# Kernel tuning notes

Hardware: AMD Instinct MI355X
Metric: run time of the kernel (lower is better)

Reference implementation:

```python
import jax, jax.numpy as jnp
import numpy as np

N, D = 16384, 64


def setup_inputs() -> dict:
    key = jax.random.key(0)
    k1, k2, k3, k4, k5 = jax.random.split(key, 5)
    x = jax.random.normal(k1, (N, D), dtype=jnp.float32)
    # labels in {-1, +1}
    y = jnp.sign(jax.random.normal(k2, (N,), dtype=jnp.float32))
    y = jnp.where(y == 0, 1.0, y)
    alpha = jax.random.uniform(k3, (N, 1), dtype=jnp.float32)
    xi = jax.random.uniform(k4, (N, 1), dtype=jnp.float32)
    b = jax.random.uniform(k5, (1,), dtype=jnp.float32, minval=-1.0, maxval=1.0)
    return {"x": x, "y": y, "alpha": alpha, "xi": xi, "b": b,
            "coeff": 1, "degree": 3, "C": 1, "lambd": 1}


def reference(x, y, alpha, xi, b, coeff, degree, C, lambd):
    a = jax.nn.relu(alpha)          # (N,1)
    xr = jax.nn.relu(xi)            # (N,1)
    # polynomial kernel Gram matrix: (x @ x.T + coeff)^degree  -> (N,N)
    K = (x @ x.T + coeff) ** degree
    # sum_j alpha_j * y_j * K_ij  (weighted row reduction)
    s = K @ (a * y[:, None])        # (N,1)
    left = y[:, None] * (s + b)     # (N,1)
    right = 1.0 - xr                # (N,1)
    loss = (0.5 * jnp.sum(jnp.abs(a))
            + C * jnp.sum(xr)
            + lambd * jnp.mean(left - right))
    return loss
```

## Files before the change

kernel.cpp:

```cpp
#include <hip/hip_runtime.h>

#define N_SAMP 16384
#define D_FEAT 64
#define TILE 128
#define NTILE 128
#define SPLIT 8
#define NPAIR (NTILE / 2)
#define NBLOCKS (NPAIR * SPLIT)
#define TPP (NTILE + 1)
#define SEG_BASE (TPP / SPLIT)
#define SEG_REM (TPP % SPLIT)

typedef __attribute__((ext_vector_type(8))) short bf16x8;
typedef __attribute__((ext_vector_type(4))) float f32x4;
typedef __attribute__((ext_vector_type(2))) float f32x2;
typedef __attribute__((ext_vector_type(4))) unsigned short u16x4;

typedef __attribute__((address_space(3))) unsigned lds_u32_t;
typedef const __attribute__((address_space(1))) unsigned glb_u32_t;

__device__ __forceinline__ void load16_to_lds(const void* g, void* l) {
  __builtin_amdgcn_global_load_lds((glb_u32_t*)g, (lds_u32_t*)l, 16, 0, 0);
}

__device__ __forceinline__ unsigned short f2bf_rne(float f) {
  union { float f; unsigned u; } v;
  v.f = f;
  unsigned u = v.u;
  return (unsigned short)((u + 0x7FFFu + ((u >> 16) & 1u)) >> 16);
}

__global__ __launch_bounds__(256) void prep_kernel(
    const float* __restrict__ x, const float* __restrict__ y,
    const float* __restrict__ alpha, const float* __restrict__ xi,
    unsigned short* __restrict__ xb, float4* __restrict__ psums) {
  int t = blockIdx.x * 256 + threadIdx.x;
  int base = t * 4;
  int row = base >> 6;
  float yv = y[row];
  float4 v = *(const float4*)(x + base);
  u16x4 o;
  o.x = f2bf_rne(v.x * yv);
  o.y = f2bf_rne(v.y * yv);
  o.z = f2bf_rne(v.z * yv);
  o.w = f2bf_rne(v.w * yv);
  *(u16x4*)(xb + base) = o;

  if (blockIdx.x < (N_SAMP / 256)) {
    float a = fmaxf(alpha[t], 0.0f);
    float xr = fmaxf(xi[t], 0.0f);
    float yy = y[t];
#pragma unroll
    for (int off = 32; off > 0; off >>= 1) {
      a += __shfl_down(a, off, 64);
      xr += __shfl_down(xr, off, 64);
      yy += __shfl_down(yy, off, 64);
    }
    __shared__ float ra[4], rx[4], ry[4];
    int wv = threadIdx.x >> 6;
    if ((threadIdx.x & 63) == 0) {
      ra[wv] = a;
      rx[wv] = xr;
      ry[wv] = yy;
    }
    __syncthreads();
    if (threadIdx.x == 0)
      psums[blockIdx.x] =
          make_float4(ra[0] + ra[1] + ra[2] + ra[3],
                      rx[0] + rx[1] + rx[2] + rx[3],
                      ry[0] + ry[1] + ry[2] + ry[3], 0.0f);
  }
}

__global__ __launch_bounds__(256, 2) void tile_kernel(
    const unsigned short* __restrict__ xb,
    const float* __restrict__ alpha,
    const float* __restrict__ y,
    const int* __restrict__ coeffp,
    const int* __restrict__ degp,
    float* __restrict__ partials) {
  __shared__ unsigned short smB[4][2][64 * 64];
  __shared__ float wred[4];

  const int tid = threadIdx.x;
  const int lane = tid & 63;
  const int wv = tid >> 6;
  const int wm = wv >> 1;
  const int wn = wv & 1;
  const int lr = lane & 15;
  const int q = lane >> 4;

  const int p = blockIdx.x >> 3;
  const int sb = blockIdx.x & (SPLIT - 1);
  const int i1 = p, i2 = NTILE - 1 - p;
  const int cnt1 = NTILE - p;
  const int g0 = sb * SEG_BASE + (sb < SEG_REM ? sb : SEG_REM);
  const int gcnt = SEG_BASE + (sb < SEG_REM ? 1 : 0);

  const char* xbytes = (const char*)xb;
  char* mybuf = (char*)smB + (wv << 14);

  const float fco = (float)coeffp[0];
  const int deg = degp[0];

  const int swz =
      ((lane >> 3) << 7) + (((lane & 7) ^ ((lane >> 3) & 7)) << 4);

  auto stage_wave = [&](int coltile, int k) {
    const char* gbase =
        xbytes + (((size_t)(coltile * TILE + wn * 64)) << 7) + swz;
    char* dst = mybuf + (k << 13);
#pragma unroll
    for (int L = 0; L < 8; ++L)
      load16_to_lds(gbase + (L << 10), dst + (L << 10));
  };

  f32x2 yr[4][2], ar[4][2];
  auto load_rows = [&](int ic) {
#pragma unroll
    for (int mt = 0; mt < 4; ++mt) {
      int idx = ic * TILE + wm * 64 + mt * 16 + q * 4;
      float4 yv = *(const float4*)(y + idx);
      float4 av = *(const float4*)(alpha + idx);
      yr[mt][0] = (f32x2){yv.x, yv.y};
      yr[mt][1] = (f32x2){yv.z, yv.w};
      ar[mt][0] = (f32x2){fmaxf(av.x, 0.0f), fmaxf(av.y, 0.0f)};
      ar[mt][1] = (f32x2){fmaxf(av.z, 0.0f), fmaxf(av.w, 0.0f)};
    }
  };

  bf16x8 af[4][2];
  auto read_af_g = [&](int rowtile) {
    const char* base = xbytes + (((size_t)(rowtile * TILE + wm * 64)) << 7);
#pragma unroll
    for (int mt = 0; mt < 4; ++mt) {
      int r = mt * 16 + lr;
#pragma unroll
      for (int kc = 0; kc < 2; ++kc)
        af[mt][kc] = *(const bf16x8*)(base + (r << 7) + ((kc * 4 + q) << 4));
    }
  };

  f32x2 rsum[4][2];
#pragma unroll
  for (int mt = 0; mt < 4; ++mt)
    for (int h = 0; h < 2; ++h) rsum[mt][h] = (f32x2){0.0f, 0.0f};
  float lane_total = 0.0f;

  auto flush_rsum = [&]() {
#pragma unroll
    for (int mt = 0; mt < 4; ++mt) {
      f32x2 s = rsum[mt][0] * ar[mt][0] + rsum[mt][1] * ar[mt][1];
      lane_total += s.x + s.y;
      rsum[mt][0] = (f32x2){0.0f, 0.0f};
      rsum[mt][1] = (f32x2){0.0f, 0.0f};
    }
  };

  int jfirst = (g0 < cnt1) ? (p + g0) : (i2 + (g0 - cnt1));
  stage_wave(jfirst, 0);
  int icur = (g0 < cnt1) ? i1 : i2;
  load_rows(icur);
  read_af_g(icur);

  for (int it = 0; it < gcnt; ++it) {
    int g = g0 + it;
    int i = (g < cnt1) ? i1 : i2;
    int j = (g < cnt1) ? (p + g) : (i2 + (g - cnt1));
    char* bufc = mybuf + ((it & 1) << 13);

    if (i != icur) {
      flush_rsum();
      load_rows(i);
      read_af_g(i);
      icur = i;
    }

    float ycol[4], wcol[4];
#pragma unroll
    for (int nt = 0; nt < 4; ++nt) {
      int jj = j * TILE + wn * 64 + nt * 16 + lr;
      ycol[nt] = y[jj];
      wcol[nt] = fmaxf(alpha[jj], 0.0f);
    }

    if (it + 1 < gcnt) {
      int gn = g + 1;
      int jn = (gn < cnt1) ? (p + gn) : (i2 + (gn - cnt1));
      stage_wave(jn, (it + 1) & 1);
      __builtin_amdgcn_s_waitcnt(0x0F78);
    } else {
      __builtin_amdgcn_s_waitcnt(0x0F70);
    }

    f32x4 acc[4][4];
#pragma unroll
    for (int mt = 0; mt < 4; ++mt) {
#pragma unroll
      for (int nt = 0; nt < 4; ++nt) {
        float s = ycol[nt] * fco;
        f32x2 lo = yr[mt][0] * s;
        f32x2 hi = yr[mt][1] * s;
        acc[mt][nt][0] = lo.x;
        acc[mt][nt][1] = lo.y;
        acc[mt][nt][2] = hi.x;
        acc[mt][nt][3] = hi.y;
      }
    }

#pragma unroll
    for (int kc = 0; kc < 2; ++kc) {
      bf16x8 bfr[4];
#pragma unroll
      for (int nt = 0; nt < 4; ++nt) {
        int rr = nt * 16 + lr;
        bfr[nt] = *(const bf16x8*)(bufc + (rr << 7) +
                                   (((kc * 4 + q) ^ (rr & 7)) << 4));
      }
#pragma unroll
      for (int mt = 0; mt < 4; ++mt) {
#pragma unroll
        for (int nt = 0; nt < 4; ++nt) {
          acc[mt][nt] = __builtin_amdgcn_mfma_f32_16x16x32_bf16(
              af[mt][kc], bfr[nt], acc[mt][nt], 0, 0, 0);
        }
      }
    }

    bool diagonal = (j == i);
    if (deg == 3) {
      if (diagonal) {
#pragma unroll
        for (int nt = 0; nt < 4; ++nt) {
          f32x2 cs = {0.0f, 0.0f};
#pragma unroll
          for (int mt = 0; mt < 4; ++mt) {
#pragma unroll
            for (int h = 0; h < 2; ++h) {
              f32x2 T = {acc[mt][nt][2 * h], acc[mt][nt][2 * h + 1]};
              f32x2 T2 = T * T;
              cs += T2 * T;
            }
          }
          lane_total = fmaf(cs.x + cs.y, wcol[nt], lane_total);
        }
      } else {
#pragma unroll
        for (int nt = 0; nt < 4; ++nt) {
          f32x2 cs = {0.0f, 0.0f};
#pragma unroll
          for (int mt = 0; mt < 4; ++mt) {
#pragma unroll
            for (int h = 0; h < 2; ++h) {
              f32x2 T = {acc[mt][nt][2 * h], acc[mt][nt][2 * h + 1]};
              f32x2 T2 = T * T;
              f32x2 P = T2 * T;
              cs += P;
              rsum[mt][h] += P;
            }
          }
          lane_total = fmaf(cs.x + cs.y, wcol[nt], lane_total);
        }
      }
    } else {
#pragma unroll
      for (int nt = 0; nt < 4; ++nt) {
        float cs = 0.0f;
#pragma unroll
        for (int mt = 0; mt < 4; ++mt) {
          float ys[4] = {yr[mt][0].x, yr[mt][0].y, yr[mt][1].x, yr[mt][1].y};
          float as[4] = {ar[mt][0].x, ar[mt][0].y, ar[mt][1].x, ar[mt][1].y};
#pragma unroll
          for (int rg = 0; rg < 4; ++rg) {
            float T = acc[mt][nt][rg];
            float pw = 1.0f;
            for (int d = 0; d < deg; ++d) pw *= T;
            if (!(deg & 1)) pw *= ys[rg] * ycol[nt];
            cs += pw;
            if (!diagonal) lane_total += pw * as[rg];
          }
        }
        lane_total = fmaf(cs, wcol[nt], lane_total);
      }
    }
  }

  flush_rsum();

#pragma unroll
  for (int off = 32; off > 0; off >>= 1)
    lane_total += __shfl_down(lane_total, off, 64);
  if (lane == 0) wred[wv] = lane_total;
  __syncthreads();
  if (tid == 0)
    partials[blockIdx.x] = wred[0] + wred[1] + wred[2] + wred[3];
}

__global__ __launch_bounds__(256) void finalize_kernel(
    const float* __restrict__ partials,
    const float4* __restrict__ psums,
    const float* __restrict__ bp,
    const int* __restrict__ Cp,
    const int* __restrict__ lamp,
    float* __restrict__ out) {
  double tsum = 0.0, sa = 0.0, sx = 0.0, sy = 0.0;
  for (int i = threadIdx.x; i < NBLOCKS; i += 256) tsum += (double)partials[i];
  if (threadIdx.x < (N_SAMP / 256)) {
    float4 v = psums[threadIdx.x];
    sa = (double)v.x;
    sx = (double)v.y;
    sy = (double)v.z;
  }
#pragma unroll
  for (int off = 32; off > 0; off >>= 1) {
    tsum += __shfl_down(tsum, off, 64);
    sa += __shfl_down(sa, off, 64);
    sx += __shfl_down(sx, off, 64);
    sy += __shfl_down(sy, off, 64);
  }
  __shared__ double red[4][4];
  int wv = threadIdx.x >> 6;
  if ((threadIdx.x & 63) == 0) {
    red[wv][0] = tsum;
    red[wv][1] = sa;
    red[wv][2] = sx;
    red[wv][3] = sy;
  }
  __syncthreads();
  if (threadIdx.x == 0) {
    double T = red[0][0] + red[1][0] + red[2][0] + red[3][0];
    double A = red[0][1] + red[1][1] + red[2][1] + red[3][1];
    double X = red[0][2] + red[1][2] + red[2][2] + red[3][2];
    double Y = red[0][3] + red[1][3] + red[2][3] + red[3][3];
    double b = (double)bp[0];
    double Cc = (double)Cp[0];
    double lam = (double)lamp[0];
    double mean = (T + b * Y - (double)N_SAMP + X) / (double)N_SAMP;
    out[0] = (float)(0.5 * A + Cc * X + lam * mean);
  }
}

extern "C" void kernel_launch(void* const* d_in, const int* in_sizes, int n_in,
                              void* d_out, int out_size, void* d_ws,
                              size_t ws_size, hipStream_t stream) {
  const float* x = (const float*)d_in[0];
  const float* y = (const float*)d_in[1];
  const float* alpha = (const float*)d_in[2];
  const float* xi = (const float*)d_in[3];
  const float* b = (const float*)d_in[4];
  const int* coeff = (const int*)d_in[5];
  const int* degree = (const int*)d_in[6];
  const int* C = (const int*)d_in[7];
  const int* lambd = (const int*)d_in[8];

  unsigned short* xb = (unsigned short*)d_ws;
  char* pbase = (char*)d_ws + (size_t)N_SAMP * D_FEAT * 2;
  float* partials = (float*)pbase;
  float4* psums = (float4*)(pbase + ((NBLOCKS * 4 + 255) & ~255));

  prep_kernel<<<(N_SAMP * D_FEAT) / (4 * 256), 256, 0, stream>>>(x, y, alpha,
                                                                 xi, xb, psums);

  tile_kernel<<<NBLOCKS, 256, 0, stream>>>(xb, alpha, y, coeff, degree,
                                           partials);

  finalize_kernel<<<1, 256, 0, stream>>>(partials, psums, b, C, lambd,
                                         (float*)d_out);
}
```

Baseline: 107.4 us.

## Fuse prep, tile and finalize kernels into one cooperative grid-synced kernel

After: 313.7 us. +192.2%, slower.

```diff
diff --git a/kernel.cpp b/kernel.cpp
--- a/kernel.cpp
+++ b/kernel.cpp
@@ -1,4 +1,7 @@
 #include <hip/hip_runtime.h>
+#include <hip/hip_cooperative_groups.h>
+
+namespace cg = cooperative_groups;
 
 #define N_SAMP 16384
 #define D_FEAT 64
@@ -28,6 +31,321 @@
   v.f = f;
   unsigned u = v.u;
   return (unsigned short)((u + 0x7FFFu + ((u >> 16) & 1u)) >> 16);
+}
+
+__global__ __launch_bounds__(256, 2) void fused_kernel(
+    const float* __restrict__ x, const float* __restrict__ y,
+    const float* __restrict__ alpha, const float* __restrict__ xi,
+    const float* __restrict__ bp, const int* __restrict__ coeffp,
+    const int* __restrict__ degp, const int* __restrict__ Cp,
+    const int* __restrict__ lamp, unsigned short* __restrict__ xb,
+    float4* __restrict__ psums, float* __restrict__ partials,
+    float* __restrict__ out) {
+  __shared__ unsigned short smB[4][2][64 * 64];
+  __shared__ float wred[4];
+  __shared__ float rtrip[3][4];
+  __shared__ double red[4][4];
+
+  const int tid = threadIdx.x;
+  const int bid = blockIdx.x;
+
+  {
+#pragma unroll
+    for (int half = 0; half < 2; ++half) {
+      int t = half * (NBLOCKS * 256) + bid * 256 + tid;
+      int base = t * 4;
+      int row = base >> 6;
+      float yv = y[row];
+      float4 v = *(const float4*)(x + base);
+      u16x4 o;
+      o.x = f2bf_rne(v.x * yv);
+      o.y = f2bf_rne(v.y * yv);
+      o.z = f2bf_rne(v.z * yv);
+      o.w = f2bf_rne(v.w * yv);
+      *(u16x4*)(xb + base) = o;
+    }
+    if (bid < (N_SAMP / 256)) {
+      int t = bid * 256 + tid;
+      float a = fmaxf(alpha[t], 0.0f);
+      float xr = fmaxf(xi[t], 0.0f);
+      float yy = y[t];
+#pragma unroll
+      for (int off = 32; off > 0; off >>= 1) {
+        a += __shfl_down(a, off, 64);
+        xr += __shfl_down(xr, off, 64);
+        yy += __shfl_down(yy, off, 64);
+      }
+      int wv = tid >> 6;
+      if ((tid & 63) == 0) {
+        rtrip[0][wv] = a;
+        rtrip[1][wv] = xr;
+        rtrip[2][wv] = yy;
+      }
+      __syncthreads();
+      if (tid == 0)
+        psums[bid] = make_float4(
+            rtrip[0][0] + rtrip[0][1] + rtrip[0][2] + rtrip[0][3],
+            rtrip[1][0] + rtrip[1][1] + rtrip[1][2] + rtrip[1][3],
+            rtrip[2][0] + rtrip[2][1] + rtrip[2][2] + rtrip[2][3], 0.0f);
+    }
+  }
+
+  __threadfence();
+  cg::this_grid().sync();
+
+  {
+    const int lane = tid & 63;
+    const int wv = tid >> 6;
+    const int wm = wv >> 1;
+    const int wn = wv & 1;
+    const int lr = lane & 15;
+    const int q = lane >> 4;
+
+    const int p = bid >> 3;
+    const int sb = bid & (SPLIT - 1);
+    const int i1 = p, i2 = NTILE - 1 - p;
+    const int cnt1 = NTILE - p;
+    const int g0 = sb * SEG_BASE + (sb < SEG_REM ? sb : SEG_REM);
+    const int gcnt = SEG_BASE + (sb < SEG_REM ? 1 : 0);
+
+    const char* xbytes = (const char*)xb;
+    char* mybuf = (char*)smB + (wv << 14);
+
+    const float fco = (float)coeffp[0];
+    const int deg = degp[0];
+
+    const int swz =
+        ((lane >> 3) << 7) + (((lane & 7) ^ ((lane >> 3) & 7)) << 4);
+
+    auto stage_wave = [&](int coltile, int k) {
+      const char* gbase =
+          xbytes + (((size_t)(coltile * TILE + wn * 64)) << 7) + swz;
+      char* dst = mybuf + (k << 13);
+#pragma unroll
+      for (int L = 0; L < 8; ++L)
+        load16_to_lds(gbase + (L << 10), dst + (L << 10));
+    };
+
+    f32x2 yr[4][2], ar[4][2];
+    auto load_rows = [&](int ic) {
+#pragma unroll
+      for (int mt = 0; mt < 4; ++mt) {
+        int idx = ic * TILE + wm * 64 + mt * 16 + q * 4;
+        float4 yv = *(const float4*)(y + idx);
+        float4 av = *(const float4*)(alpha + idx);
+        yr[mt][0] = (f32x2){yv.x, yv.y};
+        yr[mt][1] = (f32x2){yv.z, yv.w};
+        ar[mt][0] = (f32x2){fmaxf(av.x, 0.0f), fmaxf(av.y, 0.0f)};
+        ar[mt][1] = (f32x2){fmaxf(av.z, 0.0f), fmaxf(av.w, 0.0f)};
+      }
+    };
+
+    bf16x8 af[4][2];
+    auto read_af_g = [&](int rowtile) {
+      const char* base = xbytes + (((size_t)(rowtile * TILE + wm * 64)) << 7);
+#pragma unroll
+      for (int mt = 0; mt < 4; ++mt) {
+        int r = mt * 16 + lr;
+#pragma unroll
+        for (int kc = 0; kc < 2; ++kc)
+          af[mt][kc] = *(const bf16x8*)(base + (r << 7) + ((kc * 4 + q) << 4));
+      }
+    };
+
+    f32x2 rsum[4][2];
+#pragma unroll
+    for (int mt = 0; mt < 4; ++mt)
+      for (int h = 0; h < 2; ++h) rsum[mt][h] = (f32x2){0.0f, 0.0f};
+    float lane_total = 0.0f;
+
+    auto flush_rsum = [&]() {
+#pragma unroll
+      for (int mt = 0; mt < 4; ++mt) {
+        f32x2 s = rsum[mt][0] * ar[mt][0] + rsum[mt][1] * ar[mt][1];
+        lane_total += s.x + s.y;
+        rsum[mt][0] = (f32x2){0.0f, 0.0f};
+        rsum[mt][1] = (f32x2){0.0f, 0.0f};
+      }
+    };
+
+    int jfirst = (g0 < cnt1) ? (p + g0) : (i2 + (g0 - cnt1));
+    stage_wave(jfirst, 0);
+    int icur = (g0 < cnt1) ? i1 : i2;
+    load_rows(icur);
+    read_af_g(icur);
+
+    for (int it = 0; it < gcnt; ++it) {
+      int g = g0 + it;
+      int i = (g < cnt1) ? i1 : i2;
+      int j = (g < cnt1) ? (p + g) : (i2 + (g - cnt1));
+      char* bufc = mybuf + ((it & 1) << 13);
+
+      if (i != icur) {
+        flush_rsum();
+        load_rows(i);
+        read_af_g(i);
+        icur = i;
+      }
+
+      float ycol[4], wcol[4];
+#pragma unroll
+      for (int nt = 0; nt < 4; ++nt) {
+        int jj = j * TILE + wn * 64 + nt * 16 + lr;
+        ycol[nt] = y[jj];
+        wcol[nt] = fmaxf(alpha[jj], 0.0f);
+      }
+
+      if (it + 1 < gcnt) {
+        int gn = g + 1;
+        int jn = (gn < cnt1) ? (p + gn) : (i2 + (gn - cnt1));
+        stage_wave(jn, (it + 1) & 1);
+        __builtin_amdgcn_s_waitcnt(0x0F78);
+      } else {
+        __builtin_amdgcn_s_waitcnt(0x0F70);
+      }
+
+      f32x4 acc[4][4];
+#pragma unroll
+      for (int mt = 0; mt < 4; ++mt) {
+#pragma unroll
+        for (int nt = 0; nt < 4; ++nt) {
+          float s = ycol[nt] * fco;
+          f32x2 lo = yr[mt][0] * s;
+          f32x2 hi = yr[mt][1] * s;
+          acc[mt][nt][0] = lo.x;
+          acc[mt][nt][1] = lo.y;
+          acc[mt][nt][2] = hi.x;
+          acc[mt][nt][3] = hi.y;
+        }
+      }
+
+#pragma unroll
+      for (int kc = 0; kc < 2; ++kc) {
+        bf16x8 bfr[4];
+#pragma unroll
+        for (int nt = 0; nt < 4; ++nt) {
+          int rr = nt * 16 + lr;
+          bfr[nt] = *(const bf16x8*)(bufc + (rr << 7) +
+                                     (((kc * 4 + q) ^ (rr & 7)) << 4));
+        }
+#pragma unroll
+        for (int mt = 0; mt < 4; ++mt) {
+#pragma unroll
+          for (int nt = 0; nt < 4; ++nt) {
+            acc[mt][nt] = __builtin_amdgcn_mfma_f32_16x16x32_bf16(
+                af[mt][kc], bfr[nt], acc[mt][nt], 0, 0, 0);
+          }
+        }
+      }
+
+      bool diagonal = (j == i);
+      if (deg == 3) {
+        if (diagonal) {
+#pragma unroll
+          for (int nt = 0; nt < 4; ++nt) {
+            f32x2 cs = {0.0f, 0.0f};
+#pragma unroll
+            for (int mt = 0; mt < 4; ++mt) {
+#pragma unroll
+              for (int h = 0; h < 2; ++h) {
+                f32x2 T = {acc[mt][nt][2 * h], acc[mt][nt][2 * h + 1]};
+                f32x2 T2 = T * T;
+                cs += T2 * T;
+              }
+            }
+            lane_total = fmaf(cs.x + cs.y, wcol[nt], lane_total);
+          }
+        } else {
+#pragma unroll
+          for (int nt = 0; nt < 4; ++nt) {
+            f32x2 cs = {0.0f, 0.0f};
+#pragma unroll
+            for (int mt = 0; mt < 4; ++mt) {
+#pragma unroll
+              for (int h = 0; h < 2; ++h) {
+                f32x2 T = {acc[mt][nt][2 * h], acc[mt][nt][2 * h + 1]};
+                f32x2 T2 = T * T;
+                f32x2 P = T2 * T;
+                cs += P;
+                rsum[mt][h] += P;
+              }
+            }
+            lane_total = fmaf(cs.x + cs.y, wcol[nt], lane_total);
+          }
+        }
+      } else {
+#pragma unroll
+        for (int nt = 0; nt < 4; ++nt) {
+          float cs = 0.0f;
+#pragma unroll
+          for (int mt = 0; mt < 4; ++mt) {
+            float ys[4] = {yr[mt][0].x, yr[mt][0].y, yr[mt][1].x, yr[mt][1].y};
+            float as[4] = {ar[mt][0].x, ar[mt][0].y, ar[mt][1].x, ar[mt][1].y};
+#pragma unroll
+            for (int rg = 0; rg < 4; ++rg) {
+              float T = acc[mt][nt][rg];
+              float pw = 1.0f;
+              for (int d = 0; d < deg; ++d) pw *= T;
+              if (!(deg & 1)) pw *= ys[rg] * ycol[nt];
+              cs += pw;
+              if (!diagonal) lane_total += pw * as[rg];
+            }
+          }
+          lane_total = fmaf(cs, wcol[nt], lane_total);
+        }
+      }
+    }
+
+    flush_rsum();
+
+#pragma unroll
+    for (int off = 32; off > 0; off >>= 1)
+      lane_total += __shfl_down(lane_total, off, 64);
+    if (lane == 0) wred[wv] = lane_total;
+    __syncthreads();
+    if (tid == 0)
+      partials[bid] = wred[0] + wred[1] + wred[2] + wred[3];
+  }
+
+  __threadfence();
+  cg::this_grid().sync();
+
+  if (bid == 0) {
+    double tsum = 0.0, sa = 0.0, sx = 0.0, sy = 0.0;
+    for (int i = tid; i < NBLOCKS; i += 256) tsum += (double)partials[i];
+    if (tid < (N_SAMP / 256)) {
+      float4 v = psums[tid];
+      sa = (double)v.x;
+      sx = (double)v.y;
+      sy = (double)v.z;
+    }
+#pragma unroll
+    for (int off = 32; off > 0; off >>= 1) {
+      tsum += __shfl_down(tsum, off, 64);
+      sa += __shfl_down(sa, off, 64);
+      sx += __shfl_down(sx, off, 64);
+      sy += __shfl_down(sy, off, 64);
+    }
+    int wv = tid >> 6;
+    if ((tid & 63) == 0) {
+      red[wv][0] = tsum;
+      red[wv][1] = sa;
+      red[wv][2] = sx;
+      red[wv][3] = sy;
+    }
+    __syncthreads();
+    if (tid == 0) {
+      double T = red[0][0] + red[1][0] + red[2][0] + red[3][0];
+      double A = red[0][1] + red[1][1] + red[2][1] + red[3][1];
+      double X = red[0][2] + red[1][2] + red[2][2] + red[3][2];
+      double Y = red[0][3] + red[1][3] + red[2][3] + red[3][3];
+      double b = (double)bp[0];
+      double Cc = (double)Cp[0];
+      double lam = (double)lamp[0];
+      double mean = (T + b * Y - (double)N_SAMP + X) / (double)N_SAMP;
+      out[0] = (float)(0.5 * A + Cc * X + lam * mean);
+    }
+  }
 }
 
 __global__ __launch_bounds__(256) void prep_kernel(
@@ -357,13 +675,22 @@
   char* pbase = (char*)d_ws + (size_t)N_SAMP * D_FEAT * 2;
   float* partials = (float*)pbase;
   float4* psums = (float4*)(pbase + ((NBLOCKS * 4 + 255) & ~255));
-
-  prep_kernel<<<(N_SAMP * D_FEAT) / (4 * 256), 256, 0, stream>>>(x, y, alpha,
-                                                                 xi, xb, psums);
-
-  tile_kernel<<<NBLOCKS, 256, 0, stream>>>(xb, alpha, y, coeff, degree,
-                                           partials);
-
-  finalize_kernel<<<1, 256, 0, stream>>>(partials, psums, b, C, lambd,
-                                         (float*)d_out);
+  float* out = (float*)d_out;
+
+  void* args[] = {(void*)&x,     (void*)&y,      (void*)&alpha,
+                  (void*)&xi,    (void*)&b,      (void*)&coeff,
+                  (void*)&degree,(void*)&C,      (void*)&lambd,
+                  (void*)&xb,    (void*)&psums,  (void*)&partials,
+                  (void*)&out};
+  hipError_t err = hipLaunchCooperativeKernel(
+      (const void*)fused_kernel, dim3(NBLOCKS), dim3(256), (void**)args, 0,
+      stream);
+
+  if (err != hipSuccess) {
+    prep_kernel<<<(N_SAMP * D_FEAT) / (4 * 256), 256, 0, stream>>>(
+        x, y, alpha, xi, xb, psums);
+    tile_kernel<<<NBLOCKS, 256, 0, stream>>>(xb, alpha, y, coeff, degree,
+                                             partials);
+    finalize_kernel<<<1, 256, 0, stream>>>(partials, psums, b, C, lambd, out);
+  }
 }
```

## Prefetch next column labels/weights and stagger tile order across block halves

Applied to the files above, without the earlier changes.

Result: no change. 106.0 us, median of 2 (-1.2%).

```diff
diff --git a/kernel.cpp b/kernel.cpp
--- a/kernel.cpp
+++ b/kernel.cpp
@@ -97,6 +97,22 @@
   const int g0 = sb * SEG_BASE + (sb < SEG_REM ? sb : SEG_REM);
   const int gcnt = SEG_BASE + (sb < SEG_REM ? 1 : 0);
 
+  const int ph = ((blockIdx.x >> 8) & 1) * (gcnt >> 1);
+  auto map_g = [&](int it) {
+    int gg = it + ph;
+    if (gg >= gcnt) gg -= gcnt;
+    return g0 + gg;
+  };
+  auto g_to_ij = [&](int g, int& i, int& j) {
+    if (g < cnt1) {
+      i = i1;
+      j = p + g;
+    } else {
+      i = i2;
+      j = i2 + (g - cnt1);
+    }
+  };
+
   const char* xbytes = (const char*)xb;
   char* mybuf = (char*)smB + (wv << 14);
 
@@ -157,16 +173,25 @@
     }
   };
 
-  int jfirst = (g0 < cnt1) ? (p + g0) : (i2 + (g0 - cnt1));
+  int gfirst = map_g(0);
+  int icur, jfirst;
+  g_to_ij(gfirst, icur, jfirst);
   stage_wave(jfirst, 0);
-  int icur = (g0 < cnt1) ? i1 : i2;
+
+  float ycol[4], wcol[4];
+#pragma unroll
+  for (int nt = 0; nt < 4; ++nt) {
+    int jj = jfirst * TILE + wn * 64 + nt * 16 + lr;
+    ycol[nt] = y[jj];
+    wcol[nt] = fmaxf(alpha[jj], 0.0f);
+  }
   load_rows(icur);
   read_af_g(icur);
 
   for (int it = 0; it < gcnt; ++it) {
-    int g = g0 + it;
-    int i = (g < cnt1) ? i1 : i2;
-    int j = (g < cnt1) ? (p + g) : (i2 + (g - cnt1));
+    int g = map_g(it);
+    int i, j;
+    g_to_ij(g, i, j);
     char* bufc = mybuf + ((it & 1) << 13);
 
     if (i != icur) {
@@ -176,31 +201,40 @@
       icur = i;
     }
 
-    float ycol[4], wcol[4];
-#pragma unroll
-    for (int nt = 0; nt < 4; ++nt) {
-      int jj = j * TILE + wn * 64 + nt * 16 + lr;
-      ycol[nt] = y[jj];
-      wcol[nt] = fmaxf(alpha[jj], 0.0f);
-    }
-
-    if (it + 1 < gcnt) {
-      int gn = g + 1;
-      int jn = (gn < cnt1) ? (p + gn) : (i2 + (gn - cnt1));
+    int jnext = 0;
+    bool have_next = (it + 1 < gcnt);
+    if (have_next) {
+      int gn = map_g(it + 1);
+      int in_, jn;
+      g_to_ij(gn, in_, jn);
+      jnext = jn;
       stage_wave(jn, (it + 1) & 1);
       __builtin_amdgcn_s_waitcnt(0x0F78);
     } else {
       __builtin_amdgcn_s_waitcnt(0x0F70);
     }
 
+    float ycol_n[4], wraw_n[4];
+    if (have_next) {
+#pragma unroll
+      for (int nt = 0; nt < 4; ++nt) {
+        int jj = jnext * TILE + wn * 64 + nt * 16 + lr;
+        ycol_n[nt] = y[jj];
+        wraw_n[nt] = alpha[jj];
+      }
+    }
+
+    float ysc[4];
+#pragma unroll
+    for (int nt = 0; nt < 4; ++nt) ysc[nt] = ycol[nt] * fco;
+
     f32x4 acc[4][4];
 #pragma unroll
     for (int mt = 0; mt < 4; ++mt) {
 #pragma unroll
       for (int nt = 0; nt < 4; ++nt) {
-        float s = ycol[nt] * fco;
-        f32x2 lo = yr[mt][0] * s;
-        f32x2 hi = yr[mt][1] * s;
+        f32x2 lo = yr[mt][0] * ysc[nt];
+        f32x2 hi = yr[mt][1] * ysc[nt];
         acc[mt][nt][0] = lo.x;
         acc[mt][nt][1] = lo.y;
         acc[mt][nt][2] = hi.x;
@@ -281,6 +315,14 @@
           }
         }
         lane_total = fmaf(cs, wcol[nt], lane_total);
+      }
+    }
+
+    if (have_next) {
+#pragma unroll
+      for (int nt = 0; nt < 4; ++nt) {
+        ycol[nt] = ycol_n[nt];
+        wcol[nt] = fmaxf(wraw_n[nt], 0.0f);
       }
     }
   }
```

## Load B fragments straight from global and overlap previous tile's epilogue

Applied to the files above, without the earlier changes.

After: 111.0 us. 1.03x slower.

```diff
diff --git a/kernel.cpp b/kernel.cpp
--- a/kernel.cpp
+++ b/kernel.cpp
@@ -15,13 +15,6 @@
 typedef __attribute__((ext_vector_type(4))) float f32x4;
 typedef __attribute__((ext_vector_type(2))) float f32x2;
 typedef __attribute__((ext_vector_type(4))) unsigned short u16x4;
-
-typedef __attribute__((address_space(3))) unsigned lds_u32_t;
-typedef const __attribute__((address_space(1))) unsigned glb_u32_t;
-
-__device__ __forceinline__ void load16_to_lds(const void* g, void* l) {
-  __builtin_amdgcn_global_load_lds((glb_u32_t*)g, (lds_u32_t*)l, 16, 0, 0);
-}
 
 __device__ __forceinline__ unsigned short f2bf_rne(float f) {
   union { float f; unsigned u; } v;
@@ -79,7 +72,6 @@
     const int* __restrict__ coeffp,
     const int* __restrict__ degp,
     float* __restrict__ partials) {
-  __shared__ unsigned short smB[4][2][64 * 64];
   __shared__ float wred[4];
 
   const int tid = threadIdx.x;
@@ -97,23 +89,19 @@
   const int g0 = sb * SEG_BASE + (sb < SEG_REM ? sb : SEG_REM);
   const int gcnt = SEG_BASE + (sb < SEG_REM ? 1 : 0);
 
+  auto g_to_ij = [&](int g, int& i, int& j) {
+    if (g < cnt1) {
+      i = i1;
+      j = p + g;
+    } else {
+      i = i2;
+      j = i2 + (g - cnt1);
+    }
+  };
+
   const char* xbytes = (const char*)xb;
-  char* mybuf = (char*)smB + (wv << 14);
-
   const float fco = (float)coeffp[0];
   const int deg = degp[0];
-
-  const int swz =
-      ((lane >> 3) << 7) + (((lane & 7) ^ ((lane >> 3) & 7)) << 4);
-
-  auto stage_wave = [&](int coltile, int k) {
-    const char* gbase =
-        xbytes + (((size_t)(coltile * TILE + wn * 64)) << 7) + swz;
-    char* dst = mybuf + (k << 13);
-#pragma unroll
-    for (int L = 0; L < 8; ++L)
-      load16_to_lds(gbase + (L << 10), dst + (L << 10));
-  };
 
   f32x2 yr[4][2], ar[4][2];
   auto load_rows = [&](int ic) {
@@ -157,79 +145,14 @@
     }
   };
 
-  int jfirst = (g0 < cnt1) ? (p + g0) : (i2 + (g0 - cnt1));
-  stage_wave(jfirst, 0);
-  int icur = (g0 < cnt1) ? i1 : i2;
-  load_rows(icur);
-  read_af_g(icur);
-
-  for (int it = 0; it < gcnt; ++it) {
-    int g = g0 + it;
-    int i = (g < cnt1) ? i1 : i2;
-    int j = (g < cnt1) ? (p + g) : (i2 + (g - cnt1));
-    char* bufc = mybuf + ((it & 1) << 13);
-
-    if (i != icur) {
-      flush_rsum();
-      load_rows(i);
-      read_af_g(i);
-      icur = i;
-    }
-
-    float ycol[4], wcol[4];
-#pragma unroll
-    for (int nt = 0; nt < 4; ++nt) {
-      int jj = j * TILE + wn * 64 + nt * 16 + lr;
-      ycol[nt] = y[jj];
-      wcol[nt] = fmaxf(alpha[jj], 0.0f);
-    }
-
-    if (it + 1 < gcnt) {
-      int gn = g + 1;
-      int jn = (gn < cnt1) ? (p + gn) : (i2 + (gn - cnt1));
-      stage_wave(jn, (it + 1) & 1);
-      __builtin_amdgcn_s_waitcnt(0x0F78);
-    } else {
-      __builtin_amdgcn_s_waitcnt(0x0F70);
-    }
-
-    f32x4 acc[4][4];
-#pragma unroll
-    for (int mt = 0; mt < 4; ++mt) {
-#pragma unroll
-      for (int nt = 0; nt < 4; ++nt) {
-        float s = ycol[nt] * fco;
-        f32x2 lo = yr[mt][0] * s;
-        f32x2 hi = yr[mt][1] * s;
-        acc[mt][nt][0] = lo.x;
-        acc[mt][nt][1] = lo.y;
-        acc[mt][nt][2] = hi.x;
-        acc[mt][nt][3] = hi.y;
-      }
-    }
-
-#pragma unroll
-    for (int kc = 0; kc < 2; ++kc) {
-      bf16x8 bfr[4];
-#pragma unroll
-      for (int nt = 0; nt < 4; ++nt) {
-        int rr = nt * 16 + lr;
-        bfr[nt] = *(const bf16x8*)(bufc + (rr << 7) +
-                                   (((kc * 4 + q) ^ (rr & 7)) << 4));
-      }
-#pragma unroll
-      for (int mt = 0; mt < 4; ++mt) {
-#pragma unroll
-        for (int nt = 0; nt < 4; ++nt) {
-          acc[mt][nt] = __builtin_amdgcn_mfma_f32_16x16x32_bf16(
-              af[mt][kc], bfr[nt], acc[mt][nt], 0, 0, 0);
-        }
-      }
-    }
-
-    bool diagonal = (j == i);
+  f32x4 acc[4][4];
+  float ycolP[4], wcolP[4];
+  bool diagP = false;
+  bool have_prev = false;
+
+  auto epilogue_prev = [&]() {
     if (deg == 3) {
-      if (diagonal) {
+      if (diagP) {
 #pragma unroll
         for (int nt = 0; nt < 4; ++nt) {
           f32x2 cs = {0.0f, 0.0f};
@@ -242,7 +165,7 @@
               cs += T2 * T;
             }
           }
-          lane_total = fmaf(cs.x + cs.y, wcol[nt], lane_total);
+          lane_total = fmaf(cs.x + cs.y, wcolP[nt], lane_total);
         }
       } else {
 #pragma unroll
@@ -259,7 +182,7 @@
               rsum[mt][h] += P;
             }
           }
-          lane_total = fmaf(cs.x + cs.y, wcol[nt], lane_total);
+          lane_total = fmaf(cs.x + cs.y, wcolP[nt], lane_total);
         }
       }
     } else {
@@ -275,16 +198,99 @@
             float T = acc[mt][nt][rg];
             float pw = 1.0f;
             for (int d = 0; d < deg; ++d) pw *= T;
-            if (!(deg & 1)) pw *= ys[rg] * ycol[nt];
+            if (!(deg & 1)) pw *= ys[rg] * ycolP[nt];
             cs += pw;
-            if (!diagonal) lane_total += pw * as[rg];
+            if (!diagP) lane_total += pw * as[rg];
           }
         }
-        lane_total = fmaf(cs, wcol[nt], lane_total);
+        lane_total = fmaf(cs, wcolP[nt], lane_total);
       }
     }
-  }
-
+  };
+
+  {
+    int i0, j0;
+    g_to_ij(g0, i0, j0);
+    load_rows(i0);
+    read_af_g(i0);
+  }
+  int icur;
+  {
+    int j0;
+    g_to_ij(g0, icur, j0);
+  }
+
+  for (int it = 0; it < gcnt; ++it) {
+    int g = g0 + it;
+    int i, j;
+    g_to_ij(g, i, j);
+
+    const char* bbase = xbytes + (((size_t)(j * TILE + wn * 64)) << 7);
+    bf16x8 bfr[4][2];
+#pragma unroll
+    for (int nt = 0; nt < 4; ++nt) {
+      int rr = nt * 16 + lr;
+#pragma unroll
+      for (int kc = 0; kc < 2; ++kc)
+        bfr[nt][kc] = *(const bf16x8*)(bbase + (rr << 7) + ((kc * 4 + q) << 4));
+    }
+
+    float ycolN[4], wrawN[4];
+#pragma unroll
+    for (int nt = 0; nt < 4; ++nt) {
+      int jj = j * TILE + wn * 64 + nt * 16 + lr;
+      ycolN[nt] = y[jj];
+      wrawN[nt] = alpha[jj];
+    }
+
+    if (have_prev) epilogue_prev();
+
+    if (i != icur) {
+      flush_rsum();
+      load_rows(i);
+      read_af_g(i);
+      icur = i;
+    }
+
+    float ysc[4];
+#pragma unroll
+    for (int nt = 0; nt < 4; ++nt) ysc[nt] = ycolN[nt] * fco;
+
+#pragma unroll
+    for (int mt = 0; mt < 4; ++mt) {
+#pragma unroll
+      for (int nt = 0; nt < 4; ++nt) {
+        f32x2 lo = yr[mt][0] * ysc[nt];
+        f32x2 hi = yr[mt][1] * ysc[nt];
+        acc[mt][nt][0] = lo.x;
+        acc[mt][nt][1] = lo.y;
+        acc[mt][nt][2] = hi.x;
+        acc[mt][nt][3] = hi.y;
+      }
+    }
+
+#pragma unroll
+    for (int kc = 0; kc < 2; ++kc) {
+#pragma unroll
+      for (int mt = 0; mt < 4; ++mt) {
+#pragma unroll
+        for (int nt = 0; nt < 4; ++nt) {
+          acc[mt][nt] = __builtin_amdgcn_mfma_f32_16x16x32_bf16(
+              af[mt][kc], bfr[nt][kc], acc[mt][nt], 0, 0, 0);
+        }
+      }
+    }
+
+#pragma unroll
+    for (int nt = 0; nt < 4; ++nt) {
+      ycolP[nt] = ycolN[nt];
+      wcolP[nt] = fmaxf(wrawN[nt], 0.0f);
+    }
+    diagP = (j == i);
+    have_prev = true;
+  }
+
+  epilogue_prev();
   flush_rsum();
 
 #pragma unroll
```
